# Kernel tuning notes

Measured on AMD Instinct MI355X. Metric: run time of the kernel, lower is better.

## Reference

```python
import jax, jax.numpy as jnp
import numpy as np

NUM_GRAPHS = 1024
NODES_PER_GRAPH = 116
DEG = 32
IN_CH = 116
HID = 32
EPS = 1e-5


def setup_inputs() -> dict:
    key = jax.random.key(0)
    ks = jax.random.split(key, 16)
    N = NUM_GRAPHS * NODES_PER_GRAPH
    E = N * DEG
    x = jax.random.normal(ks[0], (N, IN_CH), dtype=jnp.float32)
    # edges stay within each graph: graph id per edge, then random src/dst node in that graph
    gid = jnp.arange(E, dtype=jnp.int64) // (NODES_PER_GRAPH * DEG)
    off = gid * NODES_PER_GRAPH
    src = off + jax.random.randint(ks[1], (E,), 0, NODES_PER_GRAPH, dtype=jnp.int64)
    dst = off + jax.random.randint(ks[2], (E,), 0, NODES_PER_GRAPH, dtype=jnp.int64)
    edge_index = jnp.stack([src, dst], axis=0)
    edge_weight = jax.random.uniform(ks[3], (E,), dtype=jnp.float32)
    batch = jnp.arange(N, dtype=jnp.int64) // NODES_PER_GRAPH
    xavier = lambda k, fi, fo: jax.random.uniform(k, (fi, fo), jnp.float32, -1.0, 1.0) * np.sqrt(6.0 / (fi + fo))
    return {
        "x": x, "edge_index": edge_index, "edge_weight": edge_weight, "batch": batch,
        "W1": xavier(ks[4], IN_CH, HID), "b1": jnp.zeros((HID,), jnp.float32),
        "g1": jnp.ones((HID,), jnp.float32), "be1": jnp.zeros((HID,), jnp.float32),
        "W2": xavier(ks[5], HID, 2 * HID), "b2": jnp.zeros((2 * HID,), jnp.float32),
        "g2": jnp.ones((2 * HID,), jnp.float32), "be2": jnp.zeros((2 * HID,), jnp.float32),
        "Wf1": xavier(ks[6], 4 * HID, HID), "bf1": jnp.zeros((HID,), jnp.float32),
        "gf": jnp.ones((HID,), jnp.float32), "bef": jnp.zeros((HID,), jnp.float32),
        "Wf2": xavier(ks[7], HID, 2), "bf2": jnp.zeros((2,), jnp.float32),
    }


def _gcn_conv(x, row, col, ew, W, b):
    """PyG GCNConv: linear -> add self-loops -> sym-normalized scatter-add -> +bias."""
    N = x.shape[0]
    h = x @ W  # [N, out]
    loop = jnp.arange(N, dtype=row.dtype)
    row_sl = jnp.concatenate([row, loop])
    col_sl = jnp.concatenate([col, loop])
    w_sl = jnp.concatenate([ew, jnp.ones((N,), ew.dtype)])
    deg = jax.ops.segment_sum(w_sl, col_sl, num_segments=N)
    dinv = jnp.where(deg > 0, jax.lax.rsqrt(deg), 0.0)
    norm = dinv[row_sl] * w_sl * dinv[col_sl]  # [E+N]
    msg = h[row_sl] * norm[:, None]            # gather + scale
    out = jax.ops.segment_sum(msg, col_sl, num_segments=N)
    return out + b


def _bn(x, g, b):
    # BatchNorm1d in training mode: biased batch stats over axis 0
    m = jnp.mean(x, axis=0)
    v = jnp.mean(jnp.square(x - m), axis=0)
    return (x - m) * jax.lax.rsqrt(v + EPS) * g + b


def reference(x, edge_index, edge_weight, batch, W1, b1, g1, be1, W2, b2, g2, be2,
              Wf1, bf1, gf, bef, Wf2, bf2):
    row, col = edge_index[0], edge_index[1]
    h = jax.nn.relu(_bn(_gcn_conv(x, row, col, edge_weight, W1, b1), g1, be1))
    h = jax.nn.relu(_bn(_gcn_conv(h, row, col, edge_weight, W2, b2), g2, be2))
    # global mean / max pool over graphs
    counts = jax.ops.segment_sum(jnp.ones((h.shape[0],), h.dtype), batch, num_segments=NUM_GRAPHS)
    x_mean = jax.ops.segment_sum(h, batch, num_segments=NUM_GRAPHS) / counts[:, None]
    x_max = jax.ops.segment_max(h, batch, num_segments=NUM_GRAPHS)
    emb = jnp.concatenate([x_mean, x_max], axis=1)  # [G, 4*HID]
    z = jax.nn.relu(_bn(emb @ Wf1 + bf1, gf, bef))  # dropout = identity (eval)
    return z @ Wf2 + bf2  # [G, num_classes]
```

## Files before the change

kernel.cpp:

```cpp
#include <hip/hip_runtime.h>

#define NPG 116
#define EPG (NPG * 32)
#define HID 32
#define HID2 64
#define EPS 1e-5f

#define AS 136
#define YSS 40
#define HPG 7424

using bf16x8 = __attribute__((ext_vector_type(8))) short;
using f32x4  = __attribute__((ext_vector_type(4))) float;

__device__ __forceinline__ unsigned short f2bf(float f) {
  union { float f; unsigned int i; } cv;
  cv.f = f;
  unsigned int x = cv.i;
  x += 0x7fff + ((x >> 16) & 1);
  return (unsigned short)(x >> 16);
}

#define MFMA16(a, b, c) __builtin_amdgcn_mfma_f32_16x16x32_bf16((a), (b), (c), 0, 0, 0)


__global__ __launch_bounds__(1024) void k_build(const int* __restrict__ ei,
                                                const float* __restrict__ ew,
                                                float* __restrict__ dinvg,
                                                float* __restrict__ buf,
                                                int N, int E) {
  __shared__ float Wf[NPG * NPG];
  __shared__ float degs[NPG];
  const int g = blockIdx.x, tid = threadIdx.x;
  const int nb = g * NPG, e0 = g * EPG;
  const int* rowp = ei;
  const int* colp = ei + E;

  int sarr[4], darr[4];
  float warr[4];
#pragma unroll
  for (int u = 0; u < 4; ++u) {
    int e = tid + u * 1024;
    bool ok = e < EPG;
    sarr[u] = ok ? rowp[e0 + e] - nb : 0;
    darr[u] = ok ? colp[e0 + e] - nb : 0;
    warr[u] = ok ? ew[e0 + e] : 0.0f;
  }
  for (int i = tid; i < NPG; i += 1024) degs[i] = 1.0f;
  { float4* p = (float4*)Wf;
    for (int i = tid; i < NPG * 29; i += 1024) p[i] = make_float4(0,0,0,0); }
  __syncthreads();

#pragma unroll
  for (int u = 0; u < 4; ++u) {
    if (tid + u * 1024 < EPG) {
      atomicAdd(&degs[darr[u]], warr[u]);
      atomicAdd(&Wf[darr[u] * NPG + sarr[u]], warr[u]);
    }
  }
  if (tid < NPG) atomicAdd(&Wf[tid * NPG + tid], 1.0f);
  __syncthreads();

  if (tid < NPG) dinvg[nb + tid] = rsqrtf(degs[tid]);
  int4* wb4 = (int4*)(buf + (size_t)g * HPG);
  for (int idx = tid; idx < NPG * 16; idx += 1024) {
    int r = idx >> 4, j8 = (idx & 15) * 8;
    float vb[8];
#pragma unroll
    for (int t = 0; t < 8; ++t) {
      int c = j8 + t;
      vb[t] = (c < NPG) ? Wf[r * NPG + c] : 0.0f;
    }
    int4 val;
    val.x = (unsigned)f2bf(vb[0]) | ((unsigned)f2bf(vb[1]) << 16);
    val.y = (unsigned)f2bf(vb[2]) | ((unsigned)f2bf(vb[3]) << 16);
    val.z = (unsigned)f2bf(vb[4]) | ((unsigned)f2bf(vb[5]) << 16);
    val.w = (unsigned)f2bf(vb[6]) | ((unsigned)f2bf(vb[7]) << 16);
    wb4[idx] = val;
  }
}

__global__ __launch_bounds__(512) void k_conv1(const float* __restrict__ x,
                                               const float* __restrict__ W1,
                                               const float* __restrict__ dinvg,
                                               const float* __restrict__ buf,
                                               float* __restrict__ h1,
                                               float* __restrict__ stats,
                                               int N) {
  __shared__ __align__(16) short W1T[HID * AS];
  __shared__ __align__(16) short L1T[HID * AS];
  __shared__ float dv[NPG];
  __shared__ float ss[HID], qs[HID];
  const int g = blockIdx.x, tid = threadIdx.x;
  const int nb = g * NPG;
  const int l = tid & 63, w = tid >> 6;
  const int rf = l & 15, kg = l >> 4;
  const int mt = w, rl = mt * 16 + rf;

  float4 xv[6];
  float xt[8];
  {
    const float* xr = x + (size_t)(nb + (rl < NPG ? rl : 0)) * NPG;
    const float4* xp4 = (const float4*)xr;
#pragma unroll
    for (int kk = 0; kk < 3; ++kk) {
      xv[2 * kk]     = xp4[kk * 8 + kg * 2];
      xv[2 * kk + 1] = xp4[kk * 8 + kg * 2 + 1];
    }
#pragma unroll
    for (int j = 0; j < 8; ++j) {
      int k = 96 + kg * 8 + j;
      xt[j] = (k < NPG) ? xr[k] : 0.0f;
    }
  }
  if (tid < HID) { ss[tid] = 0.0f; qs[tid] = 0.0f; }
  for (int i = tid; i < NPG; i += 512) dv[i] = dinvg[nb + i];
  for (int i = tid; i < HID * 20; i += 512) {
    int c = i / 20, k = 116 + (i - 20 * (i / 20));
    W1T[c * AS + k] = 0;
    L1T[c * AS + k] = 0;
  }
  for (int i = tid; i < NPG * HID; i += 512) {
    int k = i >> 5, c = i & 31;
    W1T[c * AS + k] = (short)f2bf(W1[i]);
  }
  __syncthreads();

  {
    f32x4 a0 = {0.f,0.f,0.f,0.f}, a1 = {0.f,0.f,0.f,0.f};
#pragma unroll
    for (int kk = 0; kk < 4; ++kk) {
      bf16x8 a;
      if (rl < NPG) {
        if (kk < 3) {
          float4 v0 = xv[2 * kk], v1 = xv[2 * kk + 1];
          a[0] = (short)f2bf(v0.x); a[1] = (short)f2bf(v0.y);
          a[2] = (short)f2bf(v0.z); a[3] = (short)f2bf(v0.w);
          a[4] = (short)f2bf(v1.x); a[5] = (short)f2bf(v1.y);
          a[6] = (short)f2bf(v1.z); a[7] = (short)f2bf(v1.w);
        } else {
#pragma unroll
          for (int j = 0; j < 8; ++j) a[j] = (short)f2bf(xt[j]);
        }
      } else {
#pragma unroll
        for (int j = 0; j < 8; ++j) a[j] = 0;
      }
      bf16x8 b0 = *(const bf16x8*)&W1T[rf * AS + kk * 32 + kg * 8];
      bf16x8 b1 = *(const bf16x8*)&W1T[(16 + rf) * AS + kk * 32 + kg * 8];
      a0 = MFMA16(a, b0, a0);
      a1 = MFMA16(a, b1, a1);
    }
#pragma unroll
    for (int i = 0; i < 4; ++i) {
      int row = mt * 16 + kg * 4 + i;
      if (row < NPG) {
        float dr = dv[row];
        L1T[rf * AS + row] = (short)f2bf(dr * a0[i]);
        L1T[(16 + rf) * AS + row] = (short)f2bf(dr * a1[i]);
      }
    }
  }
  bf16x8 av[4];
  {
    const unsigned short* wbs =
        (const unsigned short*)(buf + (size_t)g * HPG);
    const int rs = (rl < NPG ? rl : 0) * 128;
#pragma unroll
    for (int kk = 0; kk < 4; ++kk)
      av[kk] = *(const bf16x8*)&wbs[rs + kk * 32 + kg * 8];
    if (rl >= NPG) {
#pragma unroll
      for (int kk = 0; kk < 4; ++kk)
#pragma unroll
        for (int j = 0; j < 8; ++j) av[kk][j] = 0;
    }
  }
  __syncthreads();

  {
    f32x4 a0 = {0.f,0.f,0.f,0.f}, a1 = {0.f,0.f,0.f,0.f};
#pragma unroll
    for (int kk = 0; kk < 4; ++kk) {
      bf16x8 b0 = *(const bf16x8*)&L1T[rf * AS + kk * 32 + kg * 8];
      bf16x8 b1 = *(const bf16x8*)&L1T[(16 + rf) * AS + kk * 32 + kg * 8];
      a0 = MFMA16(av[kk], b0, a0);
      a1 = MFMA16(av[kk], b1, a1);
    }
    float s0 = 0.f, q0 = 0.f, s1 = 0.f, q1 = 0.f;
#pragma unroll
    for (int i = 0; i < 4; ++i) {
      int row = mt * 16 + kg * 4 + i;
      if (row < NPG) {
        float dr = dv[row];
        float v0 = dr * a0[i], v1 = dr * a1[i];
        float* hrow = h1 + (size_t)(nb + row) * HID;
        hrow[rf] = v0;
        hrow[16 + rf] = v1;
        s0 += v0; q0 += v0 * v0;
        s1 += v1; q1 += v1 * v1;
      }
    }
    atomicAdd(&ss[rf], s0);      atomicAdd(&qs[rf], q0);
    atomicAdd(&ss[16 + rf], s1); atomicAdd(&qs[16 + rf], q1);
  }
  __syncthreads();
  if (tid < HID) {
    atomicAdd(&stats[tid], ss[tid]);
    atomicAdd(&stats[32 + tid], qs[tid]);
  }
}

__global__ __launch_bounds__(512) void k_conv2(const float* __restrict__ h1,
                                               const float* __restrict__ W2,
                                               const float* __restrict__ g1,
                                               const float* __restrict__ be1,
                                               const float* __restrict__ stats,
                                               const float* __restrict__ dinvg,
                                               float* __restrict__ buf,
                                               float* __restrict__ stats2,
                                               float invN, int N) {
  __shared__ __align__(16) short ysb[128 * YSS];
  __shared__ __align__(16) short W2T[HID2 * YSS];
  __shared__ __align__(16) short L2T[HID2 * AS];
  __shared__ float dv[NPG];
  __shared__ float ss[HID2], qs[HID2];
  __shared__ float a1s[HID], c1s[HID];
  const int g = blockIdx.x, tid = threadIdx.x;
  const int nb = g * NPG;
  const int l = tid & 63, w = tid >> 6;
  const int rf = l & 15, kg = l >> 4;
  float* bufg = buf + (size_t)g * HPG;
  const int mt = w, rl = mt * 16 + rf;

  bf16x8 av[4];
  {
    const unsigned short* wbs = (const unsigned short*)bufg;
    const int rs = (rl < NPG ? rl : 0) * 128;
#pragma unroll
    for (int kk = 0; kk < 4; ++kk)
      av[kk] = *(const bf16x8*)&wbs[rs + kk * 32 + kg * 8];
    if (rl >= NPG) {
#pragma unroll
      for (int kk = 0; kk < 4; ++kk)
#pragma unroll
        for (int j = 0; j < 8; ++j) av[kk][j] = 0;
    }
  }
  if (tid < HID) {
    float m = stats[tid] * invN;
    float v = stats[32 + tid] * invN - m * m;
    float a = g1[tid] * rsqrtf(v + EPS);
    a1s[tid] = a;
    c1s[tid] = be1[tid] - m * a;
  }
  if (tid < HID2) { ss[tid] = 0.0f; qs[tid] = 0.0f; }
  { int* p = (int*)ysb;
    for (int i = tid; i < 128 * YSS / 2; i += 512) p[i] = 0; }
  { int* p = (int*)L2T;
    for (int i = tid; i < HID2 * AS / 2; i += 512) p[i] = 0; }
  for (int i = tid; i < HID * HID2; i += 512) {
    int k = i >> 6, c = i & 63;
    W2T[c * YSS + k] = (short)f2bf(W2[i]);
  }
  for (int i = tid; i < NPG; i += 512) dv[i] = dinvg[nb + i];
  __syncthreads();

  {
    const float4* hg = (const float4*)(h1 + (size_t)nb * HID);
    for (int i = tid; i < NPG * 8; i += 512) {
      int r = i >> 3, kc = i & 7, k0 = kc * 4;
      float4 hv = hg[i];
      float dr = dv[r];
      float y0 = dr * fmaxf(0.f, a1s[k0 + 0] * hv.x + c1s[k0 + 0]);
      float y1 = dr * fmaxf(0.f, a1s[k0 + 1] * hv.y + c1s[k0 + 1]);
      float y2 = dr * fmaxf(0.f, a1s[k0 + 2] * hv.z + c1s[k0 + 2]);
      float y3 = dr * fmaxf(0.f, a1s[k0 + 3] * hv.w + c1s[k0 + 3]);
      unsigned int* yp = (unsigned int*)&ysb[r * YSS + k0];
      yp[0] = (unsigned)f2bf(y0) | ((unsigned)f2bf(y1) << 16);
      yp[1] = (unsigned)f2bf(y2) | ((unsigned)f2bf(y3) << 16);
    }
  }
  __syncthreads();

#pragma unroll
  for (int u = 0; u < 4; ++u) {
    const int t = w + 8 * u;
    const int mt2 = t >> 2, nt = t & 3;
    bf16x8 a = *(const bf16x8*)&ysb[(mt2 * 16 + rf) * YSS + kg * 8];
    bf16x8 b = *(const bf16x8*)&W2T[(nt * 16 + rf) * YSS + kg * 8];
    f32x4 acc = {0.f, 0.f, 0.f, 0.f};
    acc = MFMA16(a, b, acc);
    const int col = nt * 16 + rf;
#pragma unroll
    for (int i = 0; i < 4; ++i) {
      int row = mt2 * 16 + kg * 4 + i;
      if (row < NPG) L2T[col * AS + row] = (short)f2bf(acc[i]);
    }
  }
  __syncthreads();

  {
    f32x4 acc[4];
#pragma unroll
    for (int nt = 0; nt < 4; ++nt) acc[nt] = (f32x4){0.f, 0.f, 0.f, 0.f};
#pragma unroll
    for (int kk = 0; kk < 4; ++kk) {
#pragma unroll
      for (int nt = 0; nt < 4; ++nt) {
        bf16x8 b = *(const bf16x8*)&L2T[(nt * 16 + rf) * AS + kk * 32 + kg * 8];
        acc[nt] = MFMA16(av[kk], b, acc[nt]);
      }
    }
#pragma unroll
    for (int nt = 0; nt < 4; ++nt) {
      const int col = nt * 16 + rf;
      float s_ = 0.f, q_ = 0.f;
#pragma unroll
      for (int i = 0; i < 4; ++i) {
        int row = mt * 16 + kg * 4 + i;
        if (row < NPG) {
          float v = dv[row] * acc[nt][i];
          bufg[row * HID2 + col] = v;
          s_ += v; q_ += v * v;
        }
      }
      atomicAdd(&ss[col], s_);
      atomicAdd(&qs[col], q_);
    }
  }
  __syncthreads();
  if (tid < HID2) {
    atomicAdd(&stats2[tid], ss[tid]);
    atomicAdd(&stats2[64 + tid], qs[tid]);
  }
}

__global__ __launch_bounds__(256) void k_pool(const float* __restrict__ buf,
                                              const float* __restrict__ g2,
                                              const float* __restrict__ be2,
                                              const float* __restrict__ stats2,
                                              const float* __restrict__ Wf1,
                                              float* __restrict__ z,
                                              float invN, int N) {
  __shared__ float4 psum4[256], pmax4[256];
  __shared__ __align__(16) float emb[128];
  __shared__ __align__(16) float a2s[HID2], c2s[HID2];
  int g = blockIdx.x, tid = threadIdx.x;
  if (tid < HID2) {
    float m = stats2[tid] * invN;
    float v = stats2[64 + tid] * invN - m * m;
    float a = g2[tid] * rsqrtf(v + EPS);
    a2s[tid] = a;
    c2s[tid] = be2[tid] - m * a;
  }
  __syncthreads();
  int c4 = tid & 15, rg = tid >> 4;
  float4 av = ((const float4*)a2s)[c4], bv = ((const float4*)c2s)[c4];
  const float4* h4 = (const float4*)(buf + (size_t)g * HPG);
  float4 s = {0.f, 0.f, 0.f, 0.f};
  float4 mx = {-1e30f, -1e30f, -1e30f, -1e30f};
  for (int n = rg; n < NPG; n += 16) {
    float4 v = h4[n * 16 + c4];
    float4 y;
    y.x = fmaxf(0.f, av.x * v.x + bv.x);
    y.y = fmaxf(0.f, av.y * v.y + bv.y);
    y.z = fmaxf(0.f, av.z * v.z + bv.z);
    y.w = fmaxf(0.f, av.w * v.w + bv.w);
    s.x += y.x; s.y += y.y; s.z += y.z; s.w += y.w;
    mx.x = fmaxf(mx.x, y.x); mx.y = fmaxf(mx.y, y.y);
    mx.z = fmaxf(mx.z, y.z); mx.w = fmaxf(mx.w, y.w);
  }
  psum4[rg * 16 + c4] = s;
  pmax4[rg * 16 + c4] = mx;
  __syncthreads();
  if (tid < 16) {
    float4 S = psum4[tid], M = pmax4[tid];
    for (int j = 1; j < 16; ++j) {
      float4 p = psum4[j * 16 + tid], q = pmax4[j * 16 + tid];
      S.x += p.x; S.y += p.y; S.z += p.z; S.w += p.w;
      M.x = fmaxf(M.x, q.x); M.y = fmaxf(M.y, q.y);
      M.z = fmaxf(M.z, q.z); M.w = fmaxf(M.w, q.w);
    }
    const float inv = 1.0f / NPG;
    ((float4*)emb)[tid] = make_float4(S.x * inv, S.y * inv, S.z * inv, S.w * inv);
    ((float4*)emb)[16 + tid] = M;
  }
  __syncthreads();
  if (tid < 32) {
    float acc = 0.0f;
#pragma unroll
    for (int k = 0; k < 128; ++k) acc += emb[k] * Wf1[k * 32 + tid];
    z[g * 32 + tid] = acc;
  }
}

__global__ __launch_bounds__(256) void k_final(const float* __restrict__ z,
                                               const float* __restrict__ gf,
                                               const float* __restrict__ bef,
                                               const float* __restrict__ Wf2,
                                               const float* __restrict__ bf2,
                                               float* __restrict__ out, int G) {
  __shared__ float ss[32], qs[32], af[32], cf[32];
  __shared__ float w2s[64], b2s[2];
  int tid = threadIdx.x;
  if (tid < 32) { ss[tid] = 0.0f; qs[tid] = 0.0f; }
  if (tid < 64) w2s[tid] = Wf2[tid];
  if (tid < 2) b2s[tid] = bf2[tid];
  __syncthreads();
  const float4* z4 = (const float4*)z;
  int n4 = G * 8;
  float4 s = {0.f, 0.f, 0.f, 0.f}, q = {0.f, 0.f, 0.f, 0.f};
  for (int i = tid; i < n4; i += 256) {
    float4 v = z4[i];
    s.x += v.x; s.y += v.y; s.z += v.z; s.w += v.w;
    q.x += v.x * v.x; q.y += v.y * v.y; q.z += v.z * v.z; q.w += v.w * v.w;
  }
  int cg = (tid & 7) * 4;
  atomicAdd(&ss[cg + 0], s.x); atomicAdd(&ss[cg + 1], s.y);
  atomicAdd(&ss[cg + 2], s.z); atomicAdd(&ss[cg + 3], s.w);
  atomicAdd(&qs[cg + 0], q.x); atomicAdd(&qs[cg + 1], q.y);
  atomicAdd(&qs[cg + 2], q.z); atomicAdd(&qs[cg + 3], q.w);
  __syncthreads();
  if (tid < 32) {
    float invG = 1.0f / G;
    float m = ss[tid] * invG;
    float v = qs[tid] * invG - m * m;
    float a = gf[tid] * rsqrtf(v + EPS);
    af[tid] = a;
    cf[tid] = bef[tid] - m * a;
  }
  __syncthreads();
  for (int g = tid; g < G; g += 256) {
    float o0 = b2s[0], o1 = b2s[1];
    const float4* zr = z4 + g * 8;
#pragma unroll
    for (int kc = 0; kc < 8; ++kc) {
      float4 v = zr[kc];
      int j = 4 * kc;
      float y;
      y = fmaxf(0.f, af[j + 0] * v.x + cf[j + 0]);
      o0 += y * w2s[2 * (j + 0)]; o1 += y * w2s[2 * (j + 0) + 1];
      y = fmaxf(0.f, af[j + 1] * v.y + cf[j + 1]);
      o0 += y * w2s[2 * (j + 1)]; o1 += y * w2s[2 * (j + 1) + 1];
      y = fmaxf(0.f, af[j + 2] * v.z + cf[j + 2]);
      o0 += y * w2s[2 * (j + 2)]; o1 += y * w2s[2 * (j + 2) + 1];
      y = fmaxf(0.f, af[j + 3] * v.w + cf[j + 3]);
      o0 += y * w2s[2 * (j + 3)]; o1 += y * w2s[2 * (j + 3) + 1];
    }
    out[g * 2] = o0;
    out[g * 2 + 1] = o1;
  }
}

extern "C" void kernel_launch(void* const* d_in, const int* in_sizes, int n_in,
                              void* d_out, int out_size, void* d_ws, size_t ws_size,
                              hipStream_t stream) {
  const float* x   = (const float*)d_in[0];
  const int*   ei  = (const int*)d_in[1];
  const float* ew  = (const float*)d_in[2];
  const float* W1  = (const float*)d_in[4];
  const float* g1  = (const float*)d_in[6];
  const float* be1 = (const float*)d_in[7];
  const float* W2  = (const float*)d_in[8];
  const float* g2  = (const float*)d_in[10];
  const float* be2 = (const float*)d_in[11];
  const float* Wf1 = (const float*)d_in[12];
  const float* gf  = (const float*)d_in[14];
  const float* bef = (const float*)d_in[15];
  const float* Wf2 = (const float*)d_in[16];
  const float* bf2 = (const float*)d_in[17];

  int N = in_sizes[3];
  int E = in_sizes[2];
  int G = N / NPG;

  float* ws    = (float*)d_ws;
  float* stats = ws;
  float* dinv  = ws + 256;
  float* h1    = dinv + N;
  float* buf   = h1 + (size_t)N * HID;
  float* z     = buf + (size_t)G * HPG;
  float* out   = (float*)d_out;
  float invN   = 1.0f / (float)N;

  hipMemsetAsync(stats, 0, 256 * sizeof(float), stream);
  k_build<<<G, 1024, 0, stream>>>(ei, ew, dinv, buf, N, E);
  k_conv1<<<G, 512, 0, stream>>>(x, W1, dinv, buf, h1, stats, N);
  k_conv2<<<G, 512, 0, stream>>>(h1, W2, g1, be1, stats, dinv, buf,
                                 stats + 64, invN, N);
  k_pool<<<G, 256, 0, stream>>>(buf, g2, be2, stats + 64, Wf1, z, invN, N);
  k_final<<<1, 256, 0, stream>>>(z, gf, bef, Wf2, bf2, out, G);
}
```

Before: 162.6 us.

## Hoist and vectorize global loads ahead of barriers across all kernels

Global loads (edge lists, x rows, adjacency tiles, h1, pooled activations, z) are issued as vectorized loads at kernel start and pinned in registers with empty asm, before shared-memory setup and barriers. The aim is to overlap memory latency with LDS initialization. Weight transposes now read float4, and the final kernel moves from 256 to 1024 threads. The cost is higher register pressure, and the final kernel's prefetch silently assumes G*8 fits in 8 loads per thread.

```diff
diff --git a/kernel.cpp b/kernel.cpp
--- a/kernel.cpp
+++ b/kernel.cpp
@@ -22,6 +22,10 @@
 }
 
 #define MFMA16(a, b, c) __builtin_amdgcn_mfma_f32_16x16x32_bf16((a), (b), (c), 0, 0, 0)
+
+#define KEEPF4(v) asm volatile("" :: "v"((v).x), "v"((v).y), "v"((v).z), "v"((v).w))
+#define KEEPI4(v) asm volatile("" :: "v"((v).x), "v"((v).y), "v"((v).z), "v"((v).w))
+#define KEEPB8(v) asm volatile("" :: "v"((int)(v)[0]), "v"((int)(v)[4]))
 
 
 __global__ __launch_bounds__(1024) void k_build(const int* __restrict__ ei,
@@ -33,49 +37,50 @@
   __shared__ float degs[NPG];
   const int g = blockIdx.x, tid = threadIdx.x;
   const int nb = g * NPG, e0 = g * EPG;
-  const int* rowp = ei;
-  const int* colp = ei + E;
-
-  int sarr[4], darr[4];
-  float warr[4];
-#pragma unroll
-  for (int u = 0; u < 4; ++u) {
-    int e = tid + u * 1024;
-    bool ok = e < EPG;
-    sarr[u] = ok ? rowp[e0 + e] - nb : 0;
-    darr[u] = ok ? colp[e0 + e] - nb : 0;
-    warr[u] = ok ? ew[e0 + e] : 0.0f;
+
+  int4 s4 = {0, 0, 0, 0}, d4 = {0, 0, 0, 0};
+  float4 w4 = {0.f, 0.f, 0.f, 0.f};
+  const bool has = tid < (EPG / 4);
+  if (has) {
+    s4 = ((const int4*)(ei + e0))[tid];
+    d4 = ((const int4*)(ei + E + e0))[tid];
+    w4 = ((const float4*)(ew + e0))[tid];
   }
   for (int i = tid; i < NPG; i += 1024) degs[i] = 1.0f;
   { float4* p = (float4*)Wf;
     for (int i = tid; i < NPG * 29; i += 1024) p[i] = make_float4(0,0,0,0); }
-  __syncthreads();
-
-#pragma unroll
-  for (int u = 0; u < 4; ++u) {
-    if (tid + u * 1024 < EPG) {
-      atomicAdd(&degs[darr[u]], warr[u]);
-      atomicAdd(&Wf[darr[u] * NPG + sarr[u]], warr[u]);
-    }
-  }
-  if (tid < NPG) atomicAdd(&Wf[tid * NPG + tid], 1.0f);
+  KEEPI4(s4); KEEPI4(d4); KEEPF4(w4);
+  __syncthreads();
+
+  if (has) {
+    atomicAdd(&degs[d4.x - nb], w4.x);
+    atomicAdd(&Wf[(d4.x - nb) * NPG + (s4.x - nb)], w4.x);
+    atomicAdd(&degs[d4.y - nb], w4.y);
+    atomicAdd(&Wf[(d4.y - nb) * NPG + (s4.y - nb)], w4.y);
+    atomicAdd(&degs[d4.z - nb], w4.z);
+    atomicAdd(&Wf[(d4.z - nb) * NPG + (s4.z - nb)], w4.z);
+    atomicAdd(&degs[d4.w - nb], w4.w);
+    atomicAdd(&Wf[(d4.w - nb) * NPG + (s4.w - nb)], w4.w);
+  }
+  if (tid < NPG) atomicAdd(&Wf[tid * (NPG + 1)], 1.0f);
   __syncthreads();
 
   if (tid < NPG) dinvg[nb + tid] = rsqrtf(degs[tid]);
   int4* wb4 = (int4*)(buf + (size_t)g * HPG);
   for (int idx = tid; idx < NPG * 16; idx += 1024) {
     int r = idx >> 4, j8 = (idx & 15) * 8;
-    float vb[8];
-#pragma unroll
-    for (int t = 0; t < 8; ++t) {
-      int c = j8 + t;
-      vb[t] = (c < NPG) ? Wf[r * NPG + c] : 0.0f;
+    float4 va = {0.f,0.f,0.f,0.f}, vb = {0.f,0.f,0.f,0.f};
+    if (j8 < 112) {
+      va = *(const float4*)&Wf[r * NPG + j8];
+      vb = *(const float4*)&Wf[r * NPG + j8 + 4];
+    } else if (j8 == 112) {
+      va = *(const float4*)&Wf[r * NPG + 112];
     }
     int4 val;
-    val.x = (unsigned)f2bf(vb[0]) | ((unsigned)f2bf(vb[1]) << 16);
-    val.y = (unsigned)f2bf(vb[2]) | ((unsigned)f2bf(vb[3]) << 16);
-    val.z = (unsigned)f2bf(vb[4]) | ((unsigned)f2bf(vb[5]) << 16);
-    val.w = (unsigned)f2bf(vb[6]) | ((unsigned)f2bf(vb[7]) << 16);
+    val.x = (unsigned)f2bf(va.x) | ((unsigned)f2bf(va.y) << 16);
+    val.y = (unsigned)f2bf(va.z) | ((unsigned)f2bf(va.w) << 16);
+    val.z = (unsigned)f2bf(vb.x) | ((unsigned)f2bf(vb.y) << 16);
+    val.w = (unsigned)f2bf(vb.z) | ((unsigned)f2bf(vb.w) << 16);
     wb4[idx] = val;
   }
 }
@@ -97,21 +102,30 @@
   const int rf = l & 15, kg = l >> 4;
   const int mt = w, rl = mt * 16 + rf;
 
-  float4 xv[6];
-  float xt[8];
+  float4 xv[8];
   {
     const float* xr = x + (size_t)(nb + (rl < NPG ? rl : 0)) * NPG;
-    const float4* xp4 = (const float4*)xr;
-#pragma unroll
-    for (int kk = 0; kk < 3; ++kk) {
-      xv[2 * kk]     = xp4[kk * 8 + kg * 2];
-      xv[2 * kk + 1] = xp4[kk * 8 + kg * 2 + 1];
-    }
-#pragma unroll
-    for (int j = 0; j < 8; ++j) {
-      int k = 96 + kg * 8 + j;
-      xt[j] = (k < NPG) ? xr[k] : 0.0f;
-    }
+#pragma unroll
+    for (int kk = 0; kk < 4; ++kk) {
+      int off = kk * 32 + kg * 8;
+      float4 a = {0.f,0.f,0.f,0.f}, b = {0.f,0.f,0.f,0.f};
+      if (off + 8 <= NPG) {
+        a = *(const float4*)(xr + off);
+        b = *(const float4*)(xr + off + 4);
+      } else if (off + 4 <= NPG) {
+        a = *(const float4*)(xr + off);
+      }
+      xv[2 * kk] = a;
+      xv[2 * kk + 1] = b;
+    }
+  }
+  bf16x8 av[4];
+  {
+    const unsigned short* wbs = (const unsigned short*)(buf + (size_t)g * HPG);
+    const int rs = (rl < NPG ? rl : 0) * 128;
+#pragma unroll
+    for (int kk = 0; kk < 4; ++kk)
+      av[kk] = *(const bf16x8*)&wbs[rs + kk * 32 + kg * 8];
   }
   if (tid < HID) { ss[tid] = 0.0f; qs[tid] = 0.0f; }
   for (int i = tid; i < NPG; i += 512) dv[i] = dinvg[nb + i];
@@ -120,10 +134,18 @@
     W1T[c * AS + k] = 0;
     L1T[c * AS + k] = 0;
   }
-  for (int i = tid; i < NPG * HID; i += 512) {
-    int k = i >> 5, c = i & 31;
-    W1T[c * AS + k] = (short)f2bf(W1[i]);
-  }
+  for (int i = tid; i < NPG * 8; i += 512) {
+    int k = i >> 3, c4 = (i & 7) * 4;
+    float4 v = ((const float4*)W1)[i];
+    W1T[(c4 + 0) * AS + k] = (short)f2bf(v.x);
+    W1T[(c4 + 1) * AS + k] = (short)f2bf(v.y);
+    W1T[(c4 + 2) * AS + k] = (short)f2bf(v.z);
+    W1T[(c4 + 3) * AS + k] = (short)f2bf(v.w);
+  }
+#pragma unroll
+  for (int j = 0; j < 8; ++j) { KEEPF4(xv[j]); }
+#pragma unroll
+  for (int kk = 0; kk < 4; ++kk) { KEEPB8(av[kk]); }
   __syncthreads();
 
   {
@@ -132,16 +154,11 @@
     for (int kk = 0; kk < 4; ++kk) {
       bf16x8 a;
       if (rl < NPG) {
-        if (kk < 3) {
-          float4 v0 = xv[2 * kk], v1 = xv[2 * kk + 1];
-          a[0] = (short)f2bf(v0.x); a[1] = (short)f2bf(v0.y);
-          a[2] = (short)f2bf(v0.z); a[3] = (short)f2bf(v0.w);
-          a[4] = (short)f2bf(v1.x); a[5] = (short)f2bf(v1.y);
-          a[6] = (short)f2bf(v1.z); a[7] = (short)f2bf(v1.w);
-        } else {
-#pragma unroll
-          for (int j = 0; j < 8; ++j) a[j] = (short)f2bf(xt[j]);
-        }
+        float4 v0 = xv[2 * kk], v1 = xv[2 * kk + 1];
+        a[0] = (short)f2bf(v0.x); a[1] = (short)f2bf(v0.y);
+        a[2] = (short)f2bf(v0.z); a[3] = (short)f2bf(v0.w);
+        a[4] = (short)f2bf(v1.x); a[5] = (short)f2bf(v1.y);
+        a[6] = (short)f2bf(v1.z); a[7] = (short)f2bf(v1.w);
       } else {
 #pragma unroll
         for (int j = 0; j < 8; ++j) a[j] = 0;
@@ -161,31 +178,22 @@
       }
     }
   }
-  bf16x8 av[4];
-  {
-    const unsigned short* wbs =
-        (const unsigned short*)(buf + (size_t)g * HPG);
-    const int rs = (rl < NPG ? rl : 0) * 128;
-#pragma unroll
-    for (int kk = 0; kk < 4; ++kk)
-      av[kk] = *(const bf16x8*)&wbs[rs + kk * 32 + kg * 8];
-    if (rl >= NPG) {
-#pragma unroll
-      for (int kk = 0; kk < 4; ++kk)
-#pragma unroll
-        for (int j = 0; j < 8; ++j) av[kk][j] = 0;
-    }
-  }
-  __syncthreads();
-
-  {
+  __syncthreads();
+
+  {
+    const bool ok = rl < NPG;
     f32x4 a0 = {0.f,0.f,0.f,0.f}, a1 = {0.f,0.f,0.f,0.f};
 #pragma unroll
     for (int kk = 0; kk < 4; ++kk) {
+      bf16x8 a = av[kk];
+      if (!ok) {
+#pragma unroll
+        for (int j = 0; j < 8; ++j) a[j] = 0;
+      }
       bf16x8 b0 = *(const bf16x8*)&L1T[rf * AS + kk * 32 + kg * 8];
       bf16x8 b1 = *(const bf16x8*)&L1T[(16 + rf) * AS + kk * 32 + kg * 8];
-      a0 = MFMA16(av[kk], b0, a0);
-      a1 = MFMA16(av[kk], b1, a1);
+      a0 = MFMA16(a, b0, a0);
+      a1 = MFMA16(a, b1, a1);
     }
     float s0 = 0.f, q0 = 0.f, s1 = 0.f, q1 = 0.f;
 #pragma unroll
@@ -240,12 +248,12 @@
 #pragma unroll
     for (int kk = 0; kk < 4; ++kk)
       av[kk] = *(const bf16x8*)&wbs[rs + kk * 32 + kg * 8];
-    if (rl >= NPG) {
-#pragma unroll
-      for (int kk = 0; kk < 4; ++kk)
-#pragma unroll
-        for (int j = 0; j < 8; ++j) av[kk][j] = 0;
-    }
+  }
+  float4 hv0 = {0.f,0.f,0.f,0.f}, hv1 = {0.f,0.f,0.f,0.f};
+  {
+    const float4* hg = (const float4*)(h1 + (size_t)nb * HID);
+    if (tid < NPG * 8) hv0 = hg[tid];
+    if (tid + 512 < NPG * 8) hv1 = hg[tid + 512];
   }
   if (tid < HID) {
     float m = stats[tid] * invN;
@@ -259,18 +267,26 @@
     for (int i = tid; i < 128 * YSS / 2; i += 512) p[i] = 0; }
   { int* p = (int*)L2T;
     for (int i = tid; i < HID2 * AS / 2; i += 512) p[i] = 0; }
-  for (int i = tid; i < HID * HID2; i += 512) {
-    int k = i >> 6, c = i & 63;
-    W2T[c * YSS + k] = (short)f2bf(W2[i]);
+  {
+    int k = tid >> 4, c4 = (tid & 15) * 4;
+    float4 v = ((const float4*)W2)[tid];
+    W2T[(c4 + 0) * YSS + k] = (short)f2bf(v.x);
+    W2T[(c4 + 1) * YSS + k] = (short)f2bf(v.y);
+    W2T[(c4 + 2) * YSS + k] = (short)f2bf(v.z);
+    W2T[(c4 + 3) * YSS + k] = (short)f2bf(v.w);
   }
   for (int i = tid; i < NPG; i += 512) dv[i] = dinvg[nb + i];
-  __syncthreads();
-
-  {
-    const float4* hg = (const float4*)(h1 + (size_t)nb * HID);
-    for (int i = tid; i < NPG * 8; i += 512) {
+#pragma unroll
+  for (int kk = 0; kk < 4; ++kk) { KEEPB8(av[kk]); }
+  KEEPF4(hv0); KEEPF4(hv1);
+  __syncthreads();
+
+#pragma unroll
+  for (int u = 0; u < 2; ++u) {
+    int i = tid + u * 512;
+    if (i < NPG * 8) {
+      float4 hv = u ? hv1 : hv0;
       int r = i >> 3, kc = i & 7, k0 = kc * 4;
-      float4 hv = hg[i];
       float dr = dv[r];
       float y0 = dr * fmaxf(0.f, a1s[k0 + 0] * hv.x + c1s[k0 + 0]);
       float y1 = dr * fmaxf(0.f, a1s[k0 + 1] * hv.y + c1s[k0 + 1]);
@@ -301,15 +317,21 @@
   __syncthreads();
 
   {
+    const bool ok = rl < NPG;
     f32x4 acc[4];
 #pragma unroll
     for (int nt = 0; nt < 4; ++nt) acc[nt] = (f32x4){0.f, 0.f, 0.f, 0.f};
 #pragma unroll
     for (int kk = 0; kk < 4; ++kk) {
+      bf16x8 a = av[kk];
+      if (!ok) {
+#pragma unroll
+        for (int j = 0; j < 8; ++j) a[j] = 0;
+      }
 #pragma unroll
       for (int nt = 0; nt < 4; ++nt) {
         bf16x8 b = *(const bf16x8*)&L2T[(nt * 16 + rf) * AS + kk * 32 + kg * 8];
-        acc[nt] = MFMA16(av[kk], b, acc[nt]);
+        acc[nt] = MFMA16(a, b, acc[nt]);
       }
     }
 #pragma unroll
@@ -347,6 +369,14 @@
   __shared__ __align__(16) float emb[128];
   __shared__ __align__(16) float a2s[HID2], c2s[HID2];
   int g = blockIdx.x, tid = threadIdx.x;
+  int c4 = tid & 15, rg = tid >> 4;
+  const float4* h4 = (const float4*)(buf + (size_t)g * HPG);
+  float4 hvv[8];
+#pragma unroll
+  for (int k = 0; k < 8; ++k) {
+    int n = rg + 16 * k;
+    hvv[k] = (n < NPG) ? h4[n * 16 + c4] : make_float4(0.f, 0.f, 0.f, 0.f);
+  }
   if (tid < HID2) {
     float m = stats2[tid] * invN;
     float v = stats2[64 + tid] * invN - m * m;
@@ -354,22 +384,26 @@
     a2s[tid] = a;
     c2s[tid] = be2[tid] - m * a;
   }
-  __syncthreads();
-  int c4 = tid & 15, rg = tid >> 4;
+#pragma unroll
+  for (int k = 0; k < 8; ++k) { KEEPF4(hvv[k]); }
+  __syncthreads();
   float4 av = ((const float4*)a2s)[c4], bv = ((const float4*)c2s)[c4];
-  const float4* h4 = (const float4*)(buf + (size_t)g * HPG);
   float4 s = {0.f, 0.f, 0.f, 0.f};
   float4 mx = {-1e30f, -1e30f, -1e30f, -1e30f};
-  for (int n = rg; n < NPG; n += 16) {
-    float4 v = h4[n * 16 + c4];
-    float4 y;
-    y.x = fmaxf(0.f, av.x * v.x + bv.x);
-    y.y = fmaxf(0.f, av.y * v.y + bv.y);
-    y.z = fmaxf(0.f, av.z * v.z + bv.z);
-    y.w = fmaxf(0.f, av.w * v.w + bv.w);
-    s.x += y.x; s.y += y.y; s.z += y.z; s.w += y.w;
-    mx.x = fmaxf(mx.x, y.x); mx.y = fmaxf(mx.y, y.y);
-    mx.z = fmaxf(mx.z, y.z); mx.w = fmaxf(mx.w, y.w);
+#pragma unroll
+  for (int k = 0; k < 8; ++k) {
+    int n = rg + 16 * k;
+    if (n < NPG) {
+      float4 v = hvv[k];
+      float4 y;
+      y.x = fmaxf(0.f, av.x * v.x + bv.x);
+      y.y = fmaxf(0.f, av.y * v.y + bv.y);
+      y.z = fmaxf(0.f, av.z * v.z + bv.z);
+      y.w = fmaxf(0.f, av.w * v.w + bv.w);
+      s.x += y.x; s.y += y.y; s.z += y.z; s.w += y.w;
+      mx.x = fmaxf(mx.x, y.x); mx.y = fmaxf(mx.y, y.y);
+      mx.z = fmaxf(mx.z, y.z); mx.w = fmaxf(mx.w, y.w);
+    }
   }
   psum4[rg * 16 + c4] = s;
   pmax4[rg * 16 + c4] = mx;
@@ -395,24 +429,33 @@
   }
 }
 
-__global__ __launch_bounds__(256) void k_final(const float* __restrict__ z,
-                                               const float* __restrict__ gf,
-                                               const float* __restrict__ bef,
-                                               const float* __restrict__ Wf2,
-                                               const float* __restrict__ bf2,
-                                               float* __restrict__ out, int G) {
+__global__ __launch_bounds__(1024) void k_final(const float* __restrict__ z,
+                                                const float* __restrict__ gf,
+                                                const float* __restrict__ bef,
+                                                const float* __restrict__ Wf2,
+                                                const float* __restrict__ bf2,
+                                                float* __restrict__ out, int G) {
   __shared__ float ss[32], qs[32], af[32], cf[32];
   __shared__ float w2s[64], b2s[2];
   int tid = threadIdx.x;
+  const float4* z4 = (const float4*)z;
+  int n4 = G * 8;
+  float4 zv[8];
+#pragma unroll
+  for (int u = 0; u < 8; ++u) {
+    int i = tid + u * 1024;
+    zv[u] = (i < n4) ? z4[i] : make_float4(0.f, 0.f, 0.f, 0.f);
+  }
   if (tid < 32) { ss[tid] = 0.0f; qs[tid] = 0.0f; }
   if (tid < 64) w2s[tid] = Wf2[tid];
   if (tid < 2) b2s[tid] = bf2[tid];
-  __syncthreads();
-  const float4* z4 = (const float4*)z;
-  int n4 = G * 8;
+#pragma unroll
+  for (int u = 0; u < 8; ++u) { KEEPF4(zv[u]); }
+  __syncthreads();
   float4 s = {0.f, 0.f, 0.f, 0.f}, q = {0.f, 0.f, 0.f, 0.f};
-  for (int i = tid; i < n4; i += 256) {
-    float4 v = z4[i];
+#pragma unroll
+  for (int u = 0; u < 8; ++u) {
+    float4 v = zv[u];
     s.x += v.x; s.y += v.y; s.z += v.z; s.w += v.w;
     q.x += v.x * v.x; q.y += v.y * v.y; q.z += v.z * v.z; q.w += v.w * v.w;
   }
@@ -431,7 +474,7 @@
     cf[tid] = bef[tid] - m * a;
   }
   __syncthreads();
-  for (int g = tid; g < G; g += 256) {
+  for (int g = tid; g < G; g += 1024) {
     float o0 = b2s[0], o1 = b2s[1];
     const float4* zr = z4 + g * 8;
 #pragma unroll
@@ -490,5 +533,5 @@
   k_conv2<<<G, 512, 0, stream>>>(h1, W2, g1, be1, stats, dinv, buf,
                                  stats + 64, invN, N);
   k_pool<<<G, 256, 0, stream>>>(buf, g2, be2, stats + 64, Wf1, z, invN, N);
-  k_final<<<1, 256, 0, stream>>>(z, gf, bef, Wf2, bf2, out, G);
-}
+  k_final<<<1, 1024, 0, stream>>>(z, gf, bef, Wf2, bf2, out, G);
+}
```

After: 179.9 us. 10.6% more time.
